# Performance work log

Hardware: AMD Instinct MI355X
Metric: run time of the kernel (lower is better)

Reference implementation:

```python
import jax, jax.numpy as jnp
import numpy as np

C = 256
C8 = C // 8


def setup_inputs() -> dict:
    key = jax.random.key(0)
    ks = jax.random.split(key, 9)
    B, H, W = 4, 64, 64
    s = 1.0 / np.sqrt(C)
    return {
        "pre_feat": jax.random.normal(ks[0], (B, C, H, W), jnp.float32),
        "post_feat": jax.random.normal(ks[1], (B, C, H, W), jnp.float32),
        "Wq": jax.random.normal(ks[2], (C8, C), jnp.float32) * s,
        "bq": jnp.zeros((C8,), jnp.float32),
        "Wk": jax.random.normal(ks[3], (C8, C), jnp.float32) * s,
        "bk": jnp.zeros((C8,), jnp.float32),
        "Wv": jax.random.normal(ks[4], (C, C), jnp.float32) * s,
        "bv": jnp.zeros((C,), jnp.float32),
        "gamma": jnp.zeros((1,), jnp.float32),
    }


def reference(pre_feat, post_feat, Wq, bq, Wk, bk, Wv, bv, gamma):
    B, Cc, H, W = pre_feat.shape
    N = H * W
    pre = pre_feat.reshape(B, Cc, N)    # (B, C, N)
    post = post_feat.reshape(B, Cc, N)
    # 1x1 convs == per-pixel linear projections
    q = jnp.einsum('dc,bcn->bdn', Wq, post) + bq[None, :, None]  # (B, C8, N)
    k = jnp.einsum('dc,bcn->bdn', Wk, pre) + bk[None, :, None]   # (B, C8, N)
    v = jnp.einsum('dc,bcn->bdn', Wv, pre) + bv[None, :, None]   # (B, C, N)
    # energy[b,i,j] = <q[b,:,i], k[b,:,j]>  (unscaled)
    energy = jnp.einsum('bdi,bdj->bij', q, k)                    # (B, N, N)
    attention = jax.nn.softmax(energy, axis=-1)
    # out[b,c,i] = sum_j v[b,c,j] * attention[b,i,j]
    out = jnp.einsum('bcj,bij->bci', v, attention).reshape(B, Cc, H, W)
    return gamma[0] * out + post_feat
```

## Files before the change

### kernel.cpp

```cpp
#include <hip/hip_runtime.h>
#include <hip/hip_bf16.h>

#define Bn 4
#define Cn 256
#define Dn 32
#define Nn 4096

typedef __bf16 bf16x8 __attribute__((ext_vector_type(8)));
typedef float f32x4 __attribute__((ext_vector_type(4)));

__device__ __forceinline__ float bf2f(unsigned short u) {
  unsigned int v = ((unsigned int)u) << 16;
  return __builtin_bit_cast(float, v);
}
__device__ __forceinline__ unsigned short f2bf(float f) {
  unsigned int v = __builtin_bit_cast(unsigned int, f);
  v += 0x7FFFu + ((v >> 16) & 1u);
  return (unsigned short)(v >> 16);
}
__device__ __forceinline__ unsigned int pk2(float a, float b) {
  union { __hip_bfloat162 h; unsigned int u; } x;
  x.h = __float22bfloat162_rn(make_float2(a, b));
  return x.u;
}
__device__ __forceinline__ bf16x8 ldfrag(const unsigned short* p) {
  return __builtin_bit_cast(bf16x8, *(const uint4*)p);
}
__device__ __forceinline__ uint4 pack8(const float* p) {
  float4 a = *(const float4*)p;
  float4 b = *(const float4*)(p + 4);
  union { unsigned int u2[4]; uint4 u; } x;
  x.u2[0] = pk2(a.x, a.y); x.u2[1] = pk2(a.z, a.w);
  x.u2[2] = pk2(b.x, b.y); x.u2[3] = pk2(b.z, b.w);
  return x.u;
}
__device__ __forceinline__ void async16(unsigned short* lds, const unsigned short* g) {
  __builtin_amdgcn_global_load_lds(
      (const __attribute__((address_space(1))) unsigned int*)g,
      (__attribute__((address_space(3))) unsigned int*)lds, 16, 0, 0);
}

__global__ __launch_bounds__(256) void wconv(
    const float* __restrict__ Wq, const float* __restrict__ Wk,
    const float* __restrict__ Wv,
    unsigned short* __restrict__ WqBf, unsigned short* __restrict__ WkBf,
    unsigned short* __restrict__ WvBf)
{
  const size_t base = ((size_t)blockIdx.x * 256 + threadIdx.x) * 8;
  if (base < 8192) {
    *(uint4*)(WqBf + base) = pack8(Wq + base);
  } else if (base < 16384) {
    *(uint4*)(WkBf + base - 8192) = pack8(Wk + base - 8192);
  } else {
    *(uint4*)(WvBf + base - 16384) = pack8(Wv + base - 16384);
  }
}

__global__ __launch_bounds__(256) void qkprep(
    const float* __restrict__ pre, const float* __restrict__ post,
    const unsigned short* __restrict__ WqBf, const float* __restrict__ bq,
    const unsigned short* __restrict__ WkBf, const float* __restrict__ bk,
    const unsigned short* __restrict__ WvBf, const float* __restrict__ bv,
    unsigned short* __restrict__ Qt, unsigned short* __restrict__ Kt,
    unsigned short* __restrict__ VBf)
{
  __shared__ __align__(16) unsigned short sV[256 * 40];

  const int tid = threadIdx.x;
  const int lane = tid & 63, w = tid >> 6;
  const int quad = lane >> 4, n16 = lane & 15;
  const int b = blockIdx.x >> 7;
  const int i0 = (blockIdx.x & 127) << 5;
  const int isub = w & 1, dh = w >> 1;
  const int i = i0 + isub * 16 + n16;

  const f32x4 zz = {0.f, 0.f, 0.f, 0.f};
  f32x4 aq = zz, ak = zz;
  f32x4 accv[8];
#pragma unroll
  for (int ct = 0; ct < 8; ct++) accv[ct] = zz;

  const float* postB = post + (size_t)b * Cn * Nn + i;
  const float* preB  = pre  + (size_t)b * Cn * Nn + i;

#pragma unroll
  for (int kc = 0; kc < 8; kc++) {
    const int c0 = kc * 32 + quad * 8;
    const float* pp = postB + (size_t)c0 * Nn;
    const float* pr = preB + (size_t)c0 * Nn;
    union { unsigned int u2[4]; bf16x8 v; } bp, bq8;
#pragma unroll
    for (int e2 = 0; e2 < 4; e2++) {
      float p0 = pp[(size_t)(2 * e2) * Nn], p1 = pp[(size_t)(2 * e2 + 1) * Nn];
      float r0 = pr[(size_t)(2 * e2) * Nn], r1 = pr[(size_t)(2 * e2 + 1) * Nn];
      bp.u2[e2] = pk2(p0, p1);
      bq8.u2[e2] = pk2(r0, r1);
    }
    bf16x8 awq = ldfrag(WqBf + (size_t)(dh * 16 + n16) * Cn + kc * 32 + quad * 8);
    bf16x8 awk = ldfrag(WkBf + (size_t)(dh * 16 + n16) * Cn + kc * 32 + quad * 8);
    aq = __builtin_amdgcn_mfma_f32_16x16x32_bf16(awq, bp.v, aq, 0, 0, 0);
    ak = __builtin_amdgcn_mfma_f32_16x16x32_bf16(awk, bq8.v, ak, 0, 0, 0);
#pragma unroll
    for (int ct = 0; ct < 8; ct++) {
      bf16x8 aw = ldfrag(WvBf + (size_t)(dh * 128 + ct * 16 + n16) * Cn + kc * 32 + quad * 8);
      accv[ct] = __builtin_amdgcn_mfma_f32_16x16x32_bf16(aw, bq8.v, accv[ct], 0, 0, 0);
    }
  }

  const float LOG2E = 1.44269504f;
  union { unsigned short s[4]; uint2 u; } oq, ok;
#pragma unroll
  for (int r = 0; r < 4; r++) {
    int d = dh * 16 + quad * 4 + r;
    oq.s[r] = f2bf((aq[r] + bq[d]) * LOG2E);
    ok.s[r] = f2bf(ak[r] + bk[d]);
  }
  *(uint2*)(Qt + ((size_t)b * Nn + i) * Dn + dh * 16 + quad * 4) = oq.u;
  *(uint2*)(Kt + ((size_t)b * Nn + i) * Dn + dh * 16 + quad * 4) = ok.u;

#pragma unroll
  for (int ct = 0; ct < 8; ct++) {
#pragma unroll
    for (int r = 0; r < 4; r++) {
      const int c = dh * 128 + ct * 16 + quad * 4 + r;
      sV[c * 40 + isub * 16 + n16] = f2bf(accv[ct][r] + bv[c]);
    }
  }
  __syncthreads();
#pragma unroll
  for (int k = 0; k < 4; k++) {
    const int slot = tid + k * 256;
    const int c = slot >> 2, seg = slot & 3;
    *(uint4*)(VBf + ((size_t)b * Cn + c) * Nn + i0 + seg * 8) =
        *(const uint4*)(sV + c * 40 + seg * 8);
  }
}

__global__ __launch_bounds__(256, 4) void flash_attn(
    const unsigned short* __restrict__ Qt, const unsigned short* __restrict__ Kt,
    const unsigned short* __restrict__ VBf,
    unsigned short* __restrict__ Opart, float* __restrict__ Lpart)
{
  __shared__ __align__(16) unsigned short sX[2][256 * 32];
  __shared__ __align__(16) unsigned short Pl[64 * 32];

  const int tid = threadIdx.x;
  const int lane = tid & 63, w = tid >> 6;
  const int quad = lane >> 4, n16 = lane & 15;
  const int b = blockIdx.x >> 8;
  const int js = (blockIdx.x >> 6) & 3;
  const int it = blockIdx.x & 63;
  const int i0 = it * 64;
  const int jbase = js * 1024;

  const bf16x8 qf = ldfrag(Qt + ((size_t)b * Nn + i0 + w * 16 + n16) * Dn + quad * 8);

  const f32x4 zz = {0.f, 0.f, 0.f, 0.f};
  f32x4 acc[4][4];
#pragma unroll
  for (int sub = 0; sub < 4; sub++)
#pragma unroll
    for (int ct = 0; ct < 4; ct++) acc[sub][ct] = zz;
  float lrow = 0.f;

  const int x3 = n16 & 3;
  const int xrd = (quad ^ x3) << 3;
  const int row32 = (w * 16 + n16) * 32;
  const int plw0 = row32 + ((((quad >> 1) + 0) ^ x3) << 3) + ((quad & 1) << 2);
  const int plw1 = row32 + ((((quad >> 1) + 2) ^ x3) << 3) + ((quad & 1) << 2);
  const unsigned short* pK = Kt + ((size_t)b * Nn + n16) * Dn + quad * 8;
  const unsigned short* vb = VBf + (size_t)b * Cn * Nn;
  size_t dmaoff[4];
#pragma unroll
  for (int k = 0; k < 4; k++) {
    const int row = (k * 4 + w) * 16 + (lane >> 2);
    dmaoff[k] = (size_t)row * Nn + (size_t)(((lane & 3) ^ ((lane >> 2) & 3)) << 3);
  }

#define S_PHASE(A0, A1, JT0)                                                  \
  {                                                                           \
    f32x4 sc0 = __builtin_amdgcn_mfma_f32_16x16x32_bf16((A0), qf, zz, 0, 0, 0); \
    f32x4 sc1 = __builtin_amdgcn_mfma_f32_16x16x32_bf16((A1), qf, zz, 0, 0, 0); \
    float q0 = exp2f(fminf(sc0[0], 101.f)), q1 = exp2f(fminf(sc0[1], 101.f)); \
    float q2 = exp2f(fminf(sc0[2], 101.f)), q3 = exp2f(fminf(sc0[3], 101.f)); \
    float q4 = exp2f(fminf(sc1[0], 101.f)), q5 = exp2f(fminf(sc1[1], 101.f)); \
    float q6 = exp2f(fminf(sc1[2], 101.f)), q7 = exp2f(fminf(sc1[3], 101.f)); \
    union { unsigned int u2[2]; uint2 u; } pka, pkb;                          \
    pka.u2[0] = pk2(q0, q1); pka.u2[1] = pk2(q2, q3);                         \
    pkb.u2[0] = pk2(q4, q5); pkb.u2[1] = pk2(q6, q7);                         \
    *(uint2*)&Pl[plw0] = pka.u;                                               \
    *(uint2*)&Pl[plw1] = pkb.u;                                               \
    float ps = (q0 + q1) + (q2 + q3) + (q4 + q5) + (q6 + q7);                 \
    ps += __shfl_xor(ps, 16);                                                 \
    ps += __shfl_xor(ps, 32);                                                 \
    lrow += ps;                                                               \
  }

  bf16x8 akf0 = ldfrag(pK + (size_t)jbase * Dn);
  bf16x8 akf1 = ldfrag(pK + (size_t)(jbase + 16) * Dn);
  __builtin_amdgcn_sched_barrier(0);
#pragma unroll
  for (int k = 0; k < 4; k++)
    async16(&sX[0][(k * 4 + w) * 512], vb + dmaoff[k] + jbase);
  __builtin_amdgcn_sched_barrier(0);
  S_PHASE(akf0, akf1, 0)

  for (int t = 0; t < 32; ++t) {
    const int cur = t & 1;
    __syncthreads();
    if (t < 31) {
      const int j0n = jbase + (t + 1) * 32;
      akf0 = ldfrag(pK + (size_t)j0n * Dn);
      akf1 = ldfrag(pK + (size_t)(j0n + 16) * Dn);
      __builtin_amdgcn_sched_barrier(0);
#pragma unroll
      for (int k = 0; k < 4; k++)
        async16(&sX[cur ^ 1][(k * 4 + w) * 512], vb + dmaoff[k] + j0n);
      __builtin_amdgcn_sched_barrier(0);
    }
    {
      const unsigned short* sXc = sX[cur];
      bf16x8 pB[4];
#pragma unroll
      for (int sub = 0; sub < 4; sub++)
        pB[sub] = ldfrag(&Pl[(sub * 16 + n16) * 32 + xrd]);
#pragma unroll
      for (int ct = 0; ct < 4; ct++) {
        bf16x8 av = ldfrag(&sXc[(w * 64 + ct * 16 + n16) * 32 + xrd]);
        acc[0][ct] = __builtin_amdgcn_mfma_f32_16x16x32_bf16(av, pB[0], acc[0][ct], 0, 0, 0);
        acc[1][ct] = __builtin_amdgcn_mfma_f32_16x16x32_bf16(av, pB[1], acc[1][ct], 0, 0, 0);
        acc[2][ct] = __builtin_amdgcn_mfma_f32_16x16x32_bf16(av, pB[2], acc[2][ct], 0, 0, 0);
        acc[3][ct] = __builtin_amdgcn_mfma_f32_16x16x32_bf16(av, pB[3], acc[3][ct], 0, 0, 0);
      }
    }
    if (t < 31) {
      asm volatile("s_waitcnt lgkmcnt(0)" ::: "memory");
      __builtin_amdgcn_s_barrier();
      __builtin_amdgcn_sched_barrier(0);
      S_PHASE(akf0, akf1, t + 1)
    }
  }
#undef S_PHASE

  const size_t pbase = (size_t)(js * 4 + b) * Nn;
  if (quad == 0) Lpart[pbase + i0 + w * 16 + n16] = lrow;
#pragma unroll
  for (int sub = 0; sub < 4; sub++) {
    const int i = i0 + sub * 16 + n16;
#pragma unroll
    for (int ct = 0; ct < 4; ct++) {
      union { unsigned int u2[2]; uint2 u; } pk;
      pk.u2[0] = pk2(acc[sub][ct][0], acc[sub][ct][1]);
      pk.u2[1] = pk2(acc[sub][ct][2], acc[sub][ct][3]);
      *(uint2*)(Opart + (pbase + i) * 256 + w * 64 + ct * 16 + quad * 4) = pk.u;
    }
  }
}

__global__ __launch_bounds__(256) void combine(
    const unsigned short* __restrict__ Opart, const float* __restrict__ Lpart,
    const float* __restrict__ post, const float* __restrict__ gamma,
    float* __restrict__ out)
{
  __shared__ float sT[64 * 65];
  __shared__ float sL[64];

  const int tid = threadIdx.x;
  const int b = blockIdx.x >> 8;
  const int rest = blockIdx.x & 255;
  const int i0 = (rest >> 2) * 64;
  const int c0 = (rest & 3) * 64;

  if (tid < 64) {
    float l = 0.f;
#pragma unroll
    for (int js = 0; js < 4; js++) l += Lpart[(size_t)(js * 4 + b) * Nn + i0 + tid];
    sL[tid] = 1.f / l;
  }
  __syncthreads();

#pragma unroll
  for (int pass = 0; pass < 2; pass++) {
    const int il = (tid >> 3) + pass * 32;
    const int c8 = (tid & 7) << 3;
    float a[8] = {0.f, 0.f, 0.f, 0.f, 0.f, 0.f, 0.f, 0.f};
#pragma unroll
    for (int js = 0; js < 4; js++) {
      uint4 uu = *(const uint4*)(Opart + ((size_t)(js * 4 + b) * Nn + i0 + il) * 256 + c0 + c8);
      const unsigned short* us = (const unsigned short*)&uu;
#pragma unroll
      for (int e = 0; e < 8; e++) a[e] += bf2f(us[e]);
    }
    const float inv = sL[il];
#pragma unroll
    for (int e = 0; e < 8; e++) sT[(c8 + e) * 65 + il] = a[e] * inv;
  }
  __syncthreads();

  const float g = gamma[0];
#pragma unroll
  for (int itr = 0; itr < 4; itr++) {
    const int slot = tid + itr * 256;
    const int cr = slot >> 4, i4 = (slot & 15) << 2;
    const size_t addr = ((size_t)b * Cn + c0 + cr) * Nn + i0 + i4;
    float4 pp = *(const float4*)(post + addr);
    float4 ov;
    ov.x = g * sT[cr * 65 + i4 + 0] + pp.x;
    ov.y = g * sT[cr * 65 + i4 + 1] + pp.y;
    ov.z = g * sT[cr * 65 + i4 + 2] + pp.z;
    ov.w = g * sT[cr * 65 + i4 + 3] + pp.w;
    *(float4*)(out + addr) = ov;
  }
}

extern "C" void kernel_launch(void* const* d_in, const int* in_sizes, int n_in,
                              void* d_out, int out_size, void* d_ws, size_t ws_size,
                              hipStream_t stream) {
  const float* pre   = (const float*)d_in[0];
  const float* post  = (const float*)d_in[1];
  const float* Wq    = (const float*)d_in[2];
  const float* bq    = (const float*)d_in[3];
  const float* Wk    = (const float*)d_in[4];
  const float* bk    = (const float*)d_in[5];
  const float* Wv    = (const float*)d_in[6];
  const float* bv    = (const float*)d_in[7];
  const float* gamma = (const float*)d_in[8];
  float* out = (float*)d_out;

  unsigned short* ws = (unsigned short*)d_ws;
  unsigned short* Qt    = ws;
  unsigned short* Kt    = Qt + (size_t)Bn * Nn * Dn;
  unsigned short* VBf   = Kt + (size_t)Bn * Nn * Dn;
  unsigned short* WqBf  = VBf + (size_t)Bn * Cn * Nn;
  unsigned short* WkBf  = WqBf + Dn * Cn;
  unsigned short* WvBf  = WkBf + Dn * Cn;
  float* Lpart = (float*)(WvBf + Cn * Cn);
  unsigned short* Opart = (unsigned short*)(Lpart + 4 * Bn * Nn);

  wconv<<<40, 256, 0, stream>>>(Wq, Wk, Wv, WqBf, WkBf, WvBf);
  qkprep<<<512, 256, 0, stream>>>(pre, post, WqBf, bq, WkBf, bk, WvBf, bv,
                                  Qt, Kt, VBf);
  flash_attn<<<1024, 256, 0, stream>>>(Qt, Kt, VBf, Opart, Lpart);
  combine<<<1024, 256, 0, stream>>>(Opart, Lpart, post, gamma, out);
}
```

Before: 186.8 us.

## Double-buffer P tile to overlap next score phase with PV MFMAs

```diff
diff --git a/kernel.cpp b/kernel.cpp
--- a/kernel.cpp
+++ b/kernel.cpp
@@ -142,7 +142,7 @@
     unsigned short* __restrict__ Opart, float* __restrict__ Lpart)
 {
   __shared__ __align__(16) unsigned short sX[2][256 * 32];
-  __shared__ __align__(16) unsigned short Pl[64 * 32];
+  __shared__ __align__(16) unsigned short Pl[2][64 * 32];
 
   const int tid = threadIdx.x;
   const int lane = tid & 63, w = tid >> 6;
@@ -163,24 +163,27 @@
     for (int ct = 0; ct < 4; ct++) acc[sub][ct] = zz;
   float lrow = 0.f;
 
-  const int x3 = n16 & 3;
-  const int xrd = (quad ^ x3) << 3;
-  const int row32 = (w * 16 + n16) * 32;
-  const int plw0 = row32 + ((((quad >> 1) + 0) ^ x3) << 3) + ((quad & 1) << 2);
-  const int plw1 = row32 + ((((quad >> 1) + 2) ^ x3) << 3) + ((quad & 1) << 2);
+  const int swz = n16 & 3;
+  const int xrd = (quad ^ swz) << 3;
+  const int plrow = (w * 16 + n16) * 32;
+  const int plw0 = plrow + ((((quad >> 1) + 0) ^ swz) << 3) + ((quad & 1) << 2);
+  const int plw1 = plrow + ((((quad >> 1) + 2) ^ swz) << 3) + ((quad & 1) << 2);
   const unsigned short* pK = Kt + ((size_t)b * Nn + n16) * Dn + quad * 8;
   const unsigned short* vb = VBf + (size_t)b * Cn * Nn;
   size_t dmaoff[4];
 #pragma unroll
   for (int k = 0; k < 4; k++) {
-    const int row = (k * 4 + w) * 16 + (lane >> 2);
-    dmaoff[k] = (size_t)row * Nn + (size_t)(((lane & 3) ^ ((lane >> 2) & 3)) << 3);
-  }
-
-#define S_PHASE(A0, A1, JT0)                                                  \
+    const int rl = lane >> 2;
+    dmaoff[k] = (size_t)((k * 4 + w) * 16 + rl) * Nn
+              + (size_t)(((lane & 3) ^ (rl & 3)) << 3);
+  }
+
+#define S_PHASE(BUF, J0)                                                      \
   {                                                                           \
-    f32x4 sc0 = __builtin_amdgcn_mfma_f32_16x16x32_bf16((A0), qf, zz, 0, 0, 0); \
-    f32x4 sc1 = __builtin_amdgcn_mfma_f32_16x16x32_bf16((A1), qf, zz, 0, 0, 0); \
+    bf16x8 ak0 = ldfrag(pK + (size_t)(J0) * Dn);                              \
+    bf16x8 ak1 = ldfrag(pK + (size_t)((J0) + 16) * Dn);                       \
+    f32x4 sc0 = __builtin_amdgcn_mfma_f32_16x16x32_bf16(ak0, qf, zz, 0, 0, 0);\
+    f32x4 sc1 = __builtin_amdgcn_mfma_f32_16x16x32_bf16(ak1, qf, zz, 0, 0, 0);\
     float q0 = exp2f(fminf(sc0[0], 101.f)), q1 = exp2f(fminf(sc0[1], 101.f)); \
     float q2 = exp2f(fminf(sc0[2], 101.f)), q3 = exp2f(fminf(sc0[3], 101.f)); \
     float q4 = exp2f(fminf(sc1[0], 101.f)), q5 = exp2f(fminf(sc1[1], 101.f)); \
@@ -188,42 +191,36 @@
     union { unsigned int u2[2]; uint2 u; } pka, pkb;                          \
     pka.u2[0] = pk2(q0, q1); pka.u2[1] = pk2(q2, q3);                         \
     pkb.u2[0] = pk2(q4, q5); pkb.u2[1] = pk2(q6, q7);                         \
-    *(uint2*)&Pl[plw0] = pka.u;                                               \
-    *(uint2*)&Pl[plw1] = pkb.u;                                               \
+    *(uint2*)&Pl[BUF][plw0] = pka.u;                                          \
+    *(uint2*)&Pl[BUF][plw1] = pkb.u;                                          \
     float ps = (q0 + q1) + (q2 + q3) + (q4 + q5) + (q6 + q7);                 \
     ps += __shfl_xor(ps, 16);                                                 \
     ps += __shfl_xor(ps, 32);                                                 \
     lrow += ps;                                                               \
   }
 
-  bf16x8 akf0 = ldfrag(pK + (size_t)jbase * Dn);
-  bf16x8 akf1 = ldfrag(pK + (size_t)(jbase + 16) * Dn);
-  __builtin_amdgcn_sched_barrier(0);
 #pragma unroll
   for (int k = 0; k < 4; k++)
     async16(&sX[0][(k * 4 + w) * 512], vb + dmaoff[k] + jbase);
-  __builtin_amdgcn_sched_barrier(0);
-  S_PHASE(akf0, akf1, 0)
+  S_PHASE(0, jbase)
+  __syncthreads();
 
   for (int t = 0; t < 32; ++t) {
-    const int cur = t & 1;
-    __syncthreads();
+    const int cur = t & 1, nxt = cur ^ 1;
     if (t < 31) {
       const int j0n = jbase + (t + 1) * 32;
-      akf0 = ldfrag(pK + (size_t)j0n * Dn);
-      akf1 = ldfrag(pK + (size_t)(j0n + 16) * Dn);
-      __builtin_amdgcn_sched_barrier(0);
 #pragma unroll
       for (int k = 0; k < 4; k++)
-        async16(&sX[cur ^ 1][(k * 4 + w) * 512], vb + dmaoff[k] + j0n);
-      __builtin_amdgcn_sched_barrier(0);
+        async16(&sX[nxt][(k * 4 + w) * 512], vb + dmaoff[k] + j0n);
+      S_PHASE(nxt, j0n)
     }
     {
       const unsigned short* sXc = sX[cur];
+      const unsigned short* Plc = Pl[cur];
       bf16x8 pB[4];
 #pragma unroll
       for (int sub = 0; sub < 4; sub++)
-        pB[sub] = ldfrag(&Pl[(sub * 16 + n16) * 32 + xrd]);
+        pB[sub] = ldfrag(&Plc[(sub * 16 + n16) * 32 + xrd]);
 #pragma unroll
       for (int ct = 0; ct < 4; ct++) {
         bf16x8 av = ldfrag(&sXc[(w * 64 + ct * 16 + n16) * 32 + xrd]);
@@ -233,12 +230,7 @@
         acc[3][ct] = __builtin_amdgcn_mfma_f32_16x16x32_bf16(av, pB[3], acc[3][ct], 0, 0, 0);
       }
     }
-    if (t < 31) {
-      asm volatile("s_waitcnt lgkmcnt(0)" ::: "memory");
-      __builtin_amdgcn_s_barrier();
-      __builtin_amdgcn_sched_barrier(0);
-      S_PHASE(akf0, akf1, t + 1)
-    }
+    if (t < 31) __syncthreads();
   }
 #undef S_PHASE
 
```

New measurement: 186.5 us. About the same (-0.2%).
